# Kernel optimization log

Hardware: AMD Instinct MI355X
Metric: run time of the kernel (lower is better)

## Reference

```python
import jax, jax.numpy as jnp
import numpy as np


def setup_inputs() -> dict:
    key = jax.random.key(0)
    ks = jax.random.split(key, 4)
    C, Cb = 256, 32  # in_channels, bottleneck = C // 8
    B, H, W = 4, 64, 64
    x = jax.random.normal(ks[0], (B, C, H, W), dtype=jnp.float32)
    Wq = jax.random.normal(ks[1], (Cb, C), dtype=jnp.float32) * 0.05
    Wk = jax.random.normal(ks[2], (Cb, C), dtype=jnp.float32) * 0.05
    Wv = jax.random.normal(ks[3], (C, C), dtype=jnp.float32) * 0.05
    return {
        "x": x,
        "Wq": Wq, "bq": jnp.zeros((Cb,), jnp.float32),
        "Wk": Wk, "bk": jnp.zeros((Cb,), jnp.float32),
        "Wv": Wv, "bv": jnp.zeros((C,), jnp.float32),
    }


def reference(x, Wq, bq, Wk, bk, Wv, bv):
    B, C, H, W = x.shape
    N = H * W
    xf = x.reshape(B, C, N)  # [B, C, N]
    # 1x1 convs == channel matmuls
    q = jnp.einsum('oc,bcn->bon', Wq, xf) + bq[None, :, None]  # [B, Cb, N]
    k = jnp.einsum('oc,bcn->bon', Wk, xf) + bk[None, :, None]  # [B, Cb, N]
    v = jnp.einsum('oc,bcn->bon', Wv, xf) + bv[None, :, None]  # [B, C, N]
    # attention[b, n, m] = sum_d q[b, d, n] * k[b, d, m]
    attn = jnp.einsum('bdn,bdm->bnm', q, k)  # [B, N, N]
    attn = jax.nn.softmax(attn, axis=-1)
    # out[b, c, n] = sum_m v[b, c, m] * attn[b, m, n]
    out = jnp.einsum('bcm,bmn->bcn', v, attn).reshape(B, C, H, W)
    return out + x
```

## Files before the change

### kernel.cpp

```cpp
#include <hip/hip_runtime.h>
#include <hip/hip_bf16.h>

#define B_  4
#define C_  256
#define CB_ 32
#define N_  4096

typedef short bf16x8 __attribute__((ext_vector_type(8)));
typedef float f32x4  __attribute__((ext_vector_type(4)));
typedef float f32x16 __attribute__((ext_vector_type(16)));

static __device__ __forceinline__ bf16x8 ld_bf8(const __hip_bfloat16* p) {
    return *reinterpret_cast<const bf16x8*>(p);
}
static __device__ __forceinline__ unsigned pk2(float a, float b) {
    union { __hip_bfloat16 h[2]; unsigned u; } z;
    z.h[0] = __float2bfloat16(a); z.h[1] = __float2bfloat16(b);
    return z.u;
}


__global__ __launch_bounds__(256) void wconv(
    const float* __restrict__ Wq, const float* __restrict__ Wk,
    const float* __restrict__ Wv, __hip_bfloat16* __restrict__ Wc)
{
    int idx = (blockIdx.x * 256 + threadIdx.x) * 4;
    if (idx >= 320 * 256) return;
    int o = idx >> 8, c = idx & 255;
    const float* src = o < 32 ? Wq + o * 256 + c
                     : o < 64 ? Wk + (o - 32) * 256 + c
                              : Wv + (o - 64) * 256 + c;
    float4 f = *reinterpret_cast<const float4*>(src);
    union { __hip_bfloat16 h[4]; uint2 u; } pk;
    pk.h[0] = __float2bfloat16(f.x); pk.h[1] = __float2bfloat16(f.y);
    pk.h[2] = __float2bfloat16(f.z); pk.h[3] = __float2bfloat16(f.w);
    *reinterpret_cast<uint2*>(Wc + idx) = pk.u;
}

__global__ __launch_bounds__(256) void qkv_gemm(
    const float* __restrict__ x, const __hip_bfloat16* __restrict__ Wc,
    const float* __restrict__ bq, const float* __restrict__ bk,
    const float* __restrict__ bv,
    __hip_bfloat16* __restrict__ q8, __hip_bfloat16* __restrict__ k8,
    __hip_bfloat16* __restrict__ v8)
{
    const int b = blockIdx.y, n0 = blockIdx.x * 32;
    const int tid = threadIdx.x, lane = tid & 63, w = tid >> 6;
    const int lg = lane >> 4, lr = lane & 15;
    __shared__ __attribute__((aligned(16))) __hip_bfloat16 T[2][32][40];
    const float* xb = x + (size_t)b * C_ * N_;

    f32x4 acc[5][2] = {};
    for (int s = 0; s < 8; ++s) {
        const int c0 = s * 32, buf = s & 1;
        {
            int cl = tid >> 3, n4 = (tid & 7) * 4;
            float4 f = *reinterpret_cast<const float4*>(
                &xb[(size_t)(c0 + cl) * N_ + n0 + n4]);
            T[buf][n4 + 0][cl] = __float2bfloat16(f.x);
            T[buf][n4 + 1][cl] = __float2bfloat16(f.y);
            T[buf][n4 + 2][cl] = __float2bfloat16(f.z);
            T[buf][n4 + 3][cl] = __float2bfloat16(f.w);
        }
        __syncthreads();
        bf16x8 bfr[2];
#pragma unroll
        for (int nf = 0; nf < 2; ++nf)
            bfr[nf] = *reinterpret_cast<const bf16x8*>(&T[buf][nf * 16 + lr][lg * 8]);
#pragma unroll
        for (int t = 0; t < 5; ++t) {
            const int of = w + 4 * t;
            bf16x8 af = ld_bf8(Wc + (size_t)(of * 16 + lr) * 256 + c0 + lg * 8);
#pragma unroll
            for (int nf = 0; nf < 2; ++nf)
                acc[t][nf] = __builtin_amdgcn_mfma_f32_16x16x32_bf16(af, bfr[nf], acc[t][nf], 0, 0, 0);
        }
        __syncthreads();
    }
#pragma unroll
    for (int t = 0; t < 5; ++t) {
        const int of = w + 4 * t, ob = of * 16 + lg * 4;
        float bias[4];
#pragma unroll
        for (int i = 0; i < 4; ++i) {
            int o = ob + i;
            bias[i] = o < 32 ? bq[o] : o < 64 ? bk[o - 32] : bv[o - 64];
        }
#pragma unroll
        for (int nf = 0; nf < 2; ++nf) {
            const int n = n0 + nf * 16 + lr;
            if (ob < 64) {
                union { __hip_bfloat16 h[4]; uint2 u; } pk;
#pragma unroll
                for (int i = 0; i < 4; ++i)
                    pk.h[i] = __float2bfloat16(acc[t][nf][i] + bias[i]);
                __hip_bfloat16* dst;
                if (ob < 32)
                    dst = q8 + ((size_t)(b * 4 + (ob >> 3)) * N_ + n) * 8 + (ob & 7);
                else {
                    const int ok = ob - 32;
                    dst = k8 + ((size_t)(b * 4 + (ok >> 3)) * N_ + n) * 8 + (ok & 7);
                }
                *reinterpret_cast<uint2*>(dst) = pk.u;
            } else {
#pragma unroll
                for (int i = 0; i < 4; ++i)
                    v8[((size_t)(b * (N_ / 8) + (n >> 3)) * C_ + (ob - 64 + i)) * 8
                       + (n & 7)] = __float2bfloat16(acc[t][nf][i] + bias[i]);
            }
        }
    }
}

__global__ __launch_bounds__(256) void row_stats_part(
    const __hip_bfloat16* __restrict__ q8, const __hip_bfloat16* __restrict__ k8,
    float* __restrict__ pM, float* __restrict__ pZ)
{
    const int m0 = blockIdx.x * 64, s = blockIdx.y, b = blockIdx.z;
    const int tid = threadIdx.x, lane = tid & 63, w = tid >> 6;
    const int lg = lane >> 4, lr = lane & 15;
    const __hip_bfloat16* q8b = q8 + (size_t)b * N_ * CB_;
    const __hip_bfloat16* k8b = k8 + (size_t)b * N_ * CB_;
    const int mrow = m0 + w * 16;
    bf16x8 qf = ld_bf8(q8b + ((size_t)lg * N_ + mrow + lr) * 8);
    float rm[4] = {-1e30f, -1e30f, -1e30f, -1e30f};
    float rz[4] = {0.f, 0.f, 0.f, 0.f};
    const f32x4 zero = {0.f, 0.f, 0.f, 0.f};
    const int nbeg = s * (N_ / 4);
    for (int n = nbeg; n < nbeg + N_ / 4; n += 64) {
        f32x4 sf[4];
#pragma unroll
        for (int nf = 0; nf < 4; ++nf) {
            bf16x8 kf = ld_bf8(k8b + ((size_t)lg * N_ + n + nf * 16 + lr) * 8);
            sf[nf] = __builtin_amdgcn_mfma_f32_16x16x32_bf16(qf, kf, zero, 0, 0, 0);
        }
#pragma unroll
        for (int i = 0; i < 4; ++i) {
            float tm = fmaxf(fmaxf(sf[0][i], sf[1][i]), fmaxf(sf[2][i], sf[3][i]));
            if (tm > rm[i]) { rz[i] *= __expf(rm[i] - tm); rm[i] = tm; }
            rz[i] += __expf(sf[0][i] - rm[i]) + __expf(sf[1][i] - rm[i]) +
                     __expf(sf[2][i] - rm[i]) + __expf(sf[3][i] - rm[i]);
        }
    }
#pragma unroll
    for (int off = 1; off < 16; off <<= 1) {
#pragma unroll
        for (int i = 0; i < 4; ++i) {
            float om = __shfl_xor(rm[i], off);
            float oz = __shfl_xor(rz[i], off);
            float nm = fmaxf(rm[i], om);
            rz[i] = rz[i] * __expf(rm[i] - nm) + oz * __expf(om - nm);
            rm[i] = nm;
        }
    }
    if (lr == 0) {
        const size_t base = ((size_t)s * B_ + b) * N_ + mrow + lg * 4;
#pragma unroll
        for (int i = 0; i < 4; ++i) { pM[base + i] = rm[i]; pZ[base + i] = rz[i]; }
    }
}

__global__ __launch_bounds__(256) void stats_combine(
    const float* __restrict__ pM, const float* __restrict__ pZ,
    float* __restrict__ rowE)
{
    const int i = blockIdx.x * 256 + threadIdx.x;
    const int BN = B_ * N_;
    float m0 = pM[i], m1 = pM[BN + i], m2 = pM[2 * BN + i], m3 = pM[3 * BN + i];
    float M = fmaxf(fmaxf(m0, m1), fmaxf(m2, m3));
    float Z = pZ[i]          * __expf(m0 - M) + pZ[BN + i]     * __expf(m1 - M)
            + pZ[2 * BN + i] * __expf(m2 - M) + pZ[3 * BN + i] * __expf(m3 - M);
    rowE[i] = M + logf(Z);
}

#define PV_BODY(qC0, qC1, vC, eC, qN0, qN1, vN, eN, qpN0, qpN1, vpN0, vpN1, epN, DO_LOAD) \
  {                                                                             \
    if (DO_LOAD) {                                                              \
      qN0 = ld_bf8(qpN0); qN1 = ld_bf8(qpN1);                                   \
      _Pragma("unroll")                                                         \
      for (int ct = 0; ct < 4; ++ct) {                                          \
        vN[ct][0] = ld_bf8(vpN0 + ct * 256);                                    \
        vN[ct][1] = ld_bf8(vpN1 + ct * 256);                                    \
      }                                                                         \
      _Pragma("unroll")                                                         \
      for (int g = 0; g < 4; ++g)                                               \
        eN[g] = *reinterpret_cast<const f32x4*>(epN + 8 * g);                   \
      qpN0 += 2048; qpN1 += 2048; vpN0 += 65536; vpN1 += 65536; epN += 256;     \
    }                                                                           \
    f32x16 sf = {};                                                             \
    sf = __builtin_amdgcn_mfma_f32_32x32x16_bf16(qC0, kB0, sf, 0, 0, 0);        \
    sf = __builtin_amdgcn_mfma_f32_32x32x16_bf16(qC1, kB1, sf, 0, 0, 0);        \
    unsigned W0 = pk2(__expf(sf[0]  - eC[0][0]), __expf(sf[1]  - eC[0][1]));    \
    unsigned W1 = pk2(__expf(sf[2]  - eC[0][2]), __expf(sf[3]  - eC[0][3]));    \
    unsigned W2 = pk2(__expf(sf[4]  - eC[1][0]), __expf(sf[5]  - eC[1][1]));    \
    unsigned W3 = pk2(__expf(sf[6]  - eC[1][2]), __expf(sf[7]  - eC[1][3]));    \
    unsigned W4 = pk2(__expf(sf[8]  - eC[2][0]), __expf(sf[9]  - eC[2][1]));    \
    unsigned W5 = pk2(__expf(sf[10] - eC[2][2]), __expf(sf[11] - eC[2][3]));    \
    unsigned W6 = pk2(__expf(sf[12] - eC[3][0]), __expf(sf[13] - eC[3][1]));    \
    unsigned W7 = pk2(__expf(sf[14] - eC[3][2]), __expf(sf[15] - eC[3][3]));    \
    asm("v_permlane32_swap_b32 %0, %1" : "+v"(W0), "+v"(W2));                   \
    asm("v_permlane32_swap_b32 %0, %1" : "+v"(W1), "+v"(W3));                   \
    asm("v_permlane32_swap_b32 %0, %1" : "+v"(W4), "+v"(W6));                   \
    asm("v_permlane32_swap_b32 %0, %1" : "+v"(W5), "+v"(W7));                   \
    union { unsigned u[4]; bf16x8 v8_; } f0, f1;                                \
    f0.u[0] = W0; f0.u[1] = W1; f0.u[2] = W2; f0.u[3] = W3;                     \
    f1.u[0] = W4; f1.u[1] = W5; f1.u[2] = W6; f1.u[3] = W7;                     \
    _Pragma("unroll")                                                           \
    for (int ct = 0; ct < 4; ++ct) {                                            \
      acc[ct] = __builtin_amdgcn_mfma_f32_32x32x16_bf16(vC[ct][0], f0.v8_, acc[ct], 0, 0, 0); \
      acc[ct] = __builtin_amdgcn_mfma_f32_32x32x16_bf16(vC[ct][1], f1.v8_, acc[ct], 0, 0, 0); \
    }                                                                           \
  }

__global__ __launch_bounds__(512) void pv_attn(
    const __hip_bfloat16* __restrict__ q8, const __hip_bfloat16* __restrict__ k8,
    const __hip_bfloat16* __restrict__ v8, const float* __restrict__ rowE,
    const float* __restrict__ x, float* __restrict__ out)
{
    const int bid = blockIdx.x;
    const int xcd = bid & 7, slot = bid >> 3;
    const int b = xcd >> 1, c0 = (xcd & 1) * 128, n0 = slot * 64;
    const int tid = threadIdx.x, lane = tid & 63, w = tid >> 6;
    const int ms = w >> 1, nf = w & 1;
    const int h = lane >> 5, l31 = lane & 31;
    const __hip_bfloat16* q8b = q8 + (size_t)b * N_ * CB_;
    const __hip_bfloat16* k8b = k8 + (size_t)b * N_ * CB_;
    const __hip_bfloat16* v8b = v8 + (size_t)b * (N_ / 8) * C_ * 8;

    const int nrow = n0 + nf * 32 + l31;
    bf16x8 kB0 = ld_bf8(k8b + ((size_t)h * N_ + nrow) * 8);
    bf16x8 kB1 = ld_bf8(k8b + ((size_t)(2 + h) * N_ + nrow) * 8);

    const __hip_bfloat16* qpA0 = q8b + ((size_t)h * N_ + ms * 32 + l31) * 8;
    const __hip_bfloat16* qpA1 = q8b + ((size_t)(2 + h) * N_ + ms * 32 + l31) * 8;
    const __hip_bfloat16* qpB0 = qpA0 + 128 * 8;
    const __hip_bfloat16* qpB1 = qpA1 + 128 * 8;
    const __hip_bfloat16* vpA0 = v8b + ((size_t)(ms * 4 + h) * C_ + c0 + l31) * 8;
    const __hip_bfloat16* vpA1 = v8b + ((size_t)(ms * 4 + 2 + h) * C_ + c0 + l31) * 8;
    const __hip_bfloat16* vpB0 = vpA0 + (size_t)16 * C_ * 8;
    const __hip_bfloat16* vpB1 = vpA1 + (size_t)16 * C_ * 8;
    const float* epA = rowE + (size_t)b * N_ + 4 * h + ms * 32;
    const float* epB = epA + 128;

    f32x16 acc[4] = {};
    bf16x8 qA0, qA1, qB0, qB1;
    bf16x8 vA[4][2], vB[4][2];
    f32x4 eA[4], eB[4];

    qA0 = ld_bf8(qpA0); qA1 = ld_bf8(qpA1);
#pragma unroll
    for (int ct = 0; ct < 4; ++ct) {
        vA[ct][0] = ld_bf8(vpA0 + ct * 256);
        vA[ct][1] = ld_bf8(vpA1 + ct * 256);
    }
#pragma unroll
    for (int g = 0; g < 4; ++g)
        eA[g] = *reinterpret_cast<const f32x4*>(epA + 8 * g);
    qpA0 += 2048; qpA1 += 2048; vpA0 += 65536; vpA1 += 65536; epA += 256;

    for (int tt = 0; tt < 15; ++tt) {
        PV_BODY(qA0, qA1, vA, eA, qB0, qB1, vB, eB, qpB0, qpB1, vpB0, vpB1, epB, true)
        PV_BODY(qB0, qB1, vB, eB, qA0, qA1, vA, eA, qpA0, qpA1, vpA0, vpA1, epA, true)
    }
    PV_BODY(qA0, qA1, vA, eA, qB0, qB1, vB, eB, qpB0, qpB1, vpB0, vpB1, epB, true)
    PV_BODY(qB0, qB1, vB, eB, qA0, qA1, vA, eA, qpA0, qpA1, vpA0, vpA1, epA, false)

    __shared__ __attribute__((aligned(16))) float R[128][68];
#pragma unroll 1
    for (int p = 3; p >= 0; --p) {
        if (ms == p) {
#pragma unroll
            for (int i = 0; i < 16; ++i) {
                const int cl = (i & 3) + 8 * (i >> 2) + 4 * h;
                const int nn = nf * 32 + l31;
#pragma unroll
                for (int ct = 0; ct < 4; ++ct) {
                    if (p == 3) R[ct * 32 + cl][nn] = acc[ct][i];
                    else        R[ct * 32 + cl][nn] += acc[ct][i];
                }
            }
        }
        __syncthreads();
    }
    const int cr = tid >> 2, n16 = (tid & 3) * 16;
#pragma unroll
    for (int j = 0; j < 4; ++j) {
        f32x4 rv = *reinterpret_cast<const f32x4*>(&R[cr][n16 + 4 * j]);
        const size_t gi = ((size_t)b * C_ + c0 + cr) * N_ + n0 + n16 + 4 * j;
        f32x4 xv = *reinterpret_cast<const f32x4*>(x + gi);
        *reinterpret_cast<f32x4*>(out + gi) = rv + xv;
    }
}

extern "C" void kernel_launch(void* const* d_in, const int* in_sizes, int n_in,
                              void* d_out, int out_size, void* d_ws, size_t ws_size,
                              hipStream_t stream)
{
    const float* x  = (const float*)d_in[0];
    const float* Wq = (const float*)d_in[1];
    const float* bq = (const float*)d_in[2];
    const float* Wk = (const float*)d_in[3];
    const float* bk = (const float*)d_in[4];
    const float* Wv = (const float*)d_in[5];
    const float* bv = (const float*)d_in[6];
    float* out = (float*)d_out;

    char* ws = (char*)d_ws;
    __hip_bfloat16* Wc   = (__hip_bfloat16*)(ws);
    __hip_bfloat16* q8   = (__hip_bfloat16*)(ws + 0x040000);
    __hip_bfloat16* k8   = (__hip_bfloat16*)(ws + 0x140000);
    float*          rowE = (float*)(ws + 0x240000);
    float*          pM   = (float*)(ws + 0x250000);
    float*          pZ   = (float*)(ws + 0x290000);
    __hip_bfloat16* v8   = (__hip_bfloat16*)(ws + 0x400000);

    wconv<<<80, 256, 0, stream>>>(Wq, Wk, Wv, Wc);
    qkv_gemm<<<dim3(N_ / 32, B_), 256, 0, stream>>>(x, Wc, bq, bk, bv, q8, k8, v8);
    row_stats_part<<<dim3(N_ / 64, 4, B_), 256, 0, stream>>>(q8, k8, pM, pZ);
    stats_combine<<<B_ * N_ / 256, 256, 0, stream>>>(pM, pZ, rowE);
    pv_attn<<<512, 512, 0, stream>>>(q8, k8, v8, rowE, x, out);
}
```

Measured before the change: 135.4 us.

## Software-pipeline QK score and PV MFMAs across tiles in pv_attn

Restructures the pv_attn main loop so that each step computes QK scores for the next tile while the PV MFMAs for the previous tile's probabilities are issued. Exp and bf16 packing of one tile then overlap with matrix-core work of another. Adds a prologue and epilogue to fill and drain the pipeline, and keeps the packed probabilities live in registers between steps. It also replaces the inline-asm permlane32 swaps with the compiler builtin so the scheduler can reorder around them. The extra live registers may raise register pressure.

```diff
diff --git a/kernel.cpp b/kernel.cpp
--- a/kernel.cpp
+++ b/kernel.cpp
@@ -7,6 +7,7 @@
 #define N_  4096
 
 typedef short bf16x8 __attribute__((ext_vector_type(8)));
+typedef int   i32x2  __attribute__((ext_vector_type(2)));
 typedef float f32x4  __attribute__((ext_vector_type(4)));
 typedef float f32x16 __attribute__((ext_vector_type(16)));
 
@@ -173,8 +174,16 @@
     rowE[i] = M + logf(Z);
 }
 
-#define PV_BODY(qC0, qC1, vC, eC, qN0, qN1, vN, eN, qpN0, qpN1, vpN0, vpN1, epN, DO_LOAD) \
+#define PIPE_BODY(qC0, qC1, vP, eC, qN0, qN1, vN, eN, qpN0, qpN1, vpN0, vpN1, epN, DO_LOAD) \
   {                                                                             \
+    f32x16 sf = {};                                                             \
+    sf = __builtin_amdgcn_mfma_f32_32x32x16_bf16(qC0, kB0, sf, 0, 0, 0);        \
+    sf = __builtin_amdgcn_mfma_f32_32x32x16_bf16(qC1, kB1, sf, 0, 0, 0);        \
+    _Pragma("unroll")                                                           \
+    for (int ct = 0; ct < 4; ++ct) {                                            \
+      acc[ct] = __builtin_amdgcn_mfma_f32_32x32x16_bf16(vP[ct][0], pf0, acc[ct], 0, 0, 0); \
+      acc[ct] = __builtin_amdgcn_mfma_f32_32x32x16_bf16(vP[ct][1], pf1, acc[ct], 0, 0, 0); \
+    }                                                                           \
     if (DO_LOAD) {                                                              \
       qN0 = ld_bf8(qpN0); qN1 = ld_bf8(qpN1);                                   \
       _Pragma("unroll")                                                         \
@@ -187,9 +196,6 @@
         eN[g] = *reinterpret_cast<const f32x4*>(epN + 8 * g);                   \
       qpN0 += 2048; qpN1 += 2048; vpN0 += 65536; vpN1 += 65536; epN += 256;     \
     }                                                                           \
-    f32x16 sf = {};                                                             \
-    sf = __builtin_amdgcn_mfma_f32_32x32x16_bf16(qC0, kB0, sf, 0, 0, 0);        \
-    sf = __builtin_amdgcn_mfma_f32_32x32x16_bf16(qC1, kB1, sf, 0, 0, 0);        \
     unsigned W0 = pk2(__expf(sf[0]  - eC[0][0]), __expf(sf[1]  - eC[0][1]));    \
     unsigned W1 = pk2(__expf(sf[2]  - eC[0][2]), __expf(sf[3]  - eC[0][3]));    \
     unsigned W2 = pk2(__expf(sf[4]  - eC[1][0]), __expf(sf[5]  - eC[1][1]));    \
@@ -198,18 +204,14 @@
     unsigned W5 = pk2(__expf(sf[10] - eC[2][2]), __expf(sf[11] - eC[2][3]));    \
     unsigned W6 = pk2(__expf(sf[12] - eC[3][0]), __expf(sf[13] - eC[3][1]));    \
     unsigned W7 = pk2(__expf(sf[14] - eC[3][2]), __expf(sf[15] - eC[3][3]));    \
-    asm("v_permlane32_swap_b32 %0, %1" : "+v"(W0), "+v"(W2));                   \
-    asm("v_permlane32_swap_b32 %0, %1" : "+v"(W1), "+v"(W3));                   \
-    asm("v_permlane32_swap_b32 %0, %1" : "+v"(W4), "+v"(W6));                   \
-    asm("v_permlane32_swap_b32 %0, %1" : "+v"(W5), "+v"(W7));                   \
-    union { unsigned u[4]; bf16x8 v8_; } f0, f1;                                \
-    f0.u[0] = W0; f0.u[1] = W1; f0.u[2] = W2; f0.u[3] = W3;                     \
-    f1.u[0] = W4; f1.u[1] = W5; f1.u[2] = W6; f1.u[3] = W7;                     \
-    _Pragma("unroll")                                                           \
-    for (int ct = 0; ct < 4; ++ct) {                                            \
-      acc[ct] = __builtin_amdgcn_mfma_f32_32x32x16_bf16(vC[ct][0], f0.v8_, acc[ct], 0, 0, 0); \
-      acc[ct] = __builtin_amdgcn_mfma_f32_32x32x16_bf16(vC[ct][1], f1.v8_, acc[ct], 0, 0, 0); \
-    }                                                                           \
+    i32x2 s02 = __builtin_amdgcn_permlane32_swap((int)W0, (int)W2, false, false);\
+    i32x2 s13 = __builtin_amdgcn_permlane32_swap((int)W1, (int)W3, false, false);\
+    i32x2 s46 = __builtin_amdgcn_permlane32_swap((int)W4, (int)W6, false, false);\
+    i32x2 s57 = __builtin_amdgcn_permlane32_swap((int)W5, (int)W7, false, false);\
+    union { int u[4]; bf16x8 v8_; } f0, f1;                                     \
+    f0.u[0] = s02[0]; f0.u[1] = s13[0]; f0.u[2] = s02[1]; f0.u[3] = s13[1];     \
+    f1.u[0] = s46[0]; f1.u[1] = s57[0]; f1.u[2] = s46[1]; f1.u[3] = s57[1];     \
+    pf0 = f0.v8_; pf1 = f1.v8_;                                                 \
   }
 
 __global__ __launch_bounds__(512) void pv_attn(
@@ -246,6 +248,7 @@
     bf16x8 qA0, qA1, qB0, qB1;
     bf16x8 vA[4][2], vB[4][2];
     f32x4 eA[4], eB[4];
+    bf16x8 pf0, pf1;
 
     qA0 = ld_bf8(qpA0); qA1 = ld_bf8(qpA1);
 #pragma unroll
@@ -258,12 +261,48 @@
         eA[g] = *reinterpret_cast<const f32x4*>(epA + 8 * g);
     qpA0 += 2048; qpA1 += 2048; vpA0 += 65536; vpA1 += 65536; epA += 256;
 
-    for (int tt = 0; tt < 15; ++tt) {
-        PV_BODY(qA0, qA1, vA, eA, qB0, qB1, vB, eB, qpB0, qpB1, vpB0, vpB1, epB, true)
-        PV_BODY(qB0, qB1, vB, eB, qA0, qA1, vA, eA, qpA0, qpA1, vpA0, vpA1, epA, true)
-    }
-    PV_BODY(qA0, qA1, vA, eA, qB0, qB1, vB, eB, qpB0, qpB1, vpB0, vpB1, epB, true)
-    PV_BODY(qB0, qB1, vB, eB, qA0, qA1, vA, eA, qpA0, qpA1, vpA0, vpA1, epA, false)
+    {
+        f32x16 sf = {};
+        sf = __builtin_amdgcn_mfma_f32_32x32x16_bf16(qA0, kB0, sf, 0, 0, 0);
+        sf = __builtin_amdgcn_mfma_f32_32x32x16_bf16(qA1, kB1, sf, 0, 0, 0);
+        unsigned W0 = pk2(__expf(sf[0]  - eA[0][0]), __expf(sf[1]  - eA[0][1]));
+        unsigned W1 = pk2(__expf(sf[2]  - eA[0][2]), __expf(sf[3]  - eA[0][3]));
+        unsigned W2 = pk2(__expf(sf[4]  - eA[1][0]), __expf(sf[5]  - eA[1][1]));
+        unsigned W3 = pk2(__expf(sf[6]  - eA[1][2]), __expf(sf[7]  - eA[1][3]));
+        unsigned W4 = pk2(__expf(sf[8]  - eA[2][0]), __expf(sf[9]  - eA[2][1]));
+        unsigned W5 = pk2(__expf(sf[10] - eA[2][2]), __expf(sf[11] - eA[2][3]));
+        unsigned W6 = pk2(__expf(sf[12] - eA[3][0]), __expf(sf[13] - eA[3][1]));
+        unsigned W7 = pk2(__expf(sf[14] - eA[3][2]), __expf(sf[15] - eA[3][3]));
+        i32x2 s02 = __builtin_amdgcn_permlane32_swap((int)W0, (int)W2, false, false);
+        i32x2 s13 = __builtin_amdgcn_permlane32_swap((int)W1, (int)W3, false, false);
+        i32x2 s46 = __builtin_amdgcn_permlane32_swap((int)W4, (int)W6, false, false);
+        i32x2 s57 = __builtin_amdgcn_permlane32_swap((int)W5, (int)W7, false, false);
+        union { int u[4]; bf16x8 v8_; } f0, f1;
+        f0.u[0] = s02[0]; f0.u[1] = s13[0]; f0.u[2] = s02[1]; f0.u[3] = s13[1];
+        f1.u[0] = s46[0]; f1.u[1] = s57[0]; f1.u[2] = s46[1]; f1.u[3] = s57[1];
+        pf0 = f0.v8_; pf1 = f1.v8_;
+    }
+    qB0 = ld_bf8(qpB0); qB1 = ld_bf8(qpB1);
+#pragma unroll
+    for (int ct = 0; ct < 4; ++ct) {
+        vB[ct][0] = ld_bf8(vpB0 + ct * 256);
+        vB[ct][1] = ld_bf8(vpB1 + ct * 256);
+    }
+#pragma unroll
+    for (int g = 0; g < 4; ++g)
+        eB[g] = *reinterpret_cast<const f32x4*>(epB + 8 * g);
+    qpB0 += 2048; qpB1 += 2048; vpB0 += 65536; vpB1 += 65536; epB += 256;
+
+    for (int it = 0; it < 15; ++it) {
+        PIPE_BODY(qB0, qB1, vA, eB, qA0, qA1, vA, eA, qpA0, qpA1, vpA0, vpA1, epA, true)
+        PIPE_BODY(qA0, qA1, vB, eA, qB0, qB1, vB, eB, qpB0, qpB1, vpB0, vpB1, epB, true)
+    }
+    PIPE_BODY(qB0, qB1, vA, eB, qA0, qA1, vA, eA, qpA0, qpA1, vpA0, vpA1, epA, false)
+#pragma unroll
+    for (int ct = 0; ct < 4; ++ct) {
+        acc[ct] = __builtin_amdgcn_mfma_f32_32x32x16_bf16(vB[ct][0], pf0, acc[ct], 0, 0, 0);
+        acc[ct] = __builtin_amdgcn_mfma_f32_32x32x16_bf16(vB[ct][1], pf1, acc[ct], 0, 0, 0);
+    }
 
     __shared__ __attribute__((aligned(16))) float R[128][68];
 #pragma unroll 1
```

Result: no change. 134.5 us (-0.6%).

## Stage V tiles through double-buffered LDS in pv_attn instead of per-wave global loads

Applied to the files above, without the earlier changes.

The PV attention kernel now loads each V tile cooperatively into a 64KB double-buffered shared-memory region and has waves read their MFMA operands from LDS. Before, each wave loaded V directly from global memory and waves sharing a channel range fetched the same data. The change also swaps the bf16 pack for a byte-permute truncation and uses the permlane32_swap builtin instead of inline asm. In exchange it adds a __syncthreads per step, uses a large LDS allocation that limits occupancy, and the bf16 conversion now truncates instead of rounding.

```diff
diff --git a/kernel.cpp b/kernel.cpp
--- a/kernel.cpp
+++ b/kernel.cpp
@@ -7,6 +7,7 @@
 #define N_  4096
 
 typedef short bf16x8 __attribute__((ext_vector_type(8)));
+typedef int   i32x2  __attribute__((ext_vector_type(2)));
 typedef float f32x4  __attribute__((ext_vector_type(4)));
 typedef float f32x16 __attribute__((ext_vector_type(16)));
 
@@ -14,9 +15,8 @@
     return *reinterpret_cast<const bf16x8*>(p);
 }
 static __device__ __forceinline__ unsigned pk2(float a, float b) {
-    union { __hip_bfloat16 h[2]; unsigned u; } z;
-    z.h[0] = __float2bfloat16(a); z.h[1] = __float2bfloat16(b);
-    return z.u;
+    return __builtin_amdgcn_perm(__float_as_uint(a), __float_as_uint(b),
+                                 0x03020706u);
 }
 
 
@@ -173,23 +173,34 @@
     rowE[i] = M + logf(Z);
 }
 
-#define PV_BODY(qC0, qC1, vC, eC, qN0, qN1, vN, eN, qpN0, qpN1, vpN0, vpN1, epN, DO_LOAD) \
+#define PV_BODY(qC0, qC1, eC, qN0, qN1, eN, qpN0, qpN1, epN, DO_LOAD)          \
   {                                                                             \
+                                    \
+    bf16x8 vC[4][2];                                                            \
+    _Pragma("unroll")                                                           \
+    for (int ct = 0; ct < 4; ++ct) {                                            \
+      vC[ct][0] = *reinterpret_cast<const bf16x8*>(LB + curoff + rb0 + ct * 512);\
+      vC[ct][1] = *reinterpret_cast<const bf16x8*>(LB + curoff + rb1 + ct * 512);\
+    }                                                                           \
+        \
+    uint4 st0, st1, st2, st3;                                                   \
     if (DO_LOAD) {                                                              \
+      st0 = *reinterpret_cast<const uint4*>(vs0);                               \
+      st1 = *reinterpret_cast<const uint4*>(vs1);                               \
+      st2 = *reinterpret_cast<const uint4*>(vs2);                               \
+      st3 = *reinterpret_cast<const uint4*>(vs3);                               \
+      vs0 += 32768; vs1 += 32768; vs2 += 32768; vs3 += 32768;                   \
       qN0 = ld_bf8(qpN0); qN1 = ld_bf8(qpN1);                                   \
-      _Pragma("unroll")                                                         \
-      for (int ct = 0; ct < 4; ++ct) {                                          \
-        vN[ct][0] = ld_bf8(vpN0 + ct * 256);                                    \
-        vN[ct][1] = ld_bf8(vpN1 + ct * 256);                                    \
-      }                                                                         \
       _Pragma("unroll")                                                         \
       for (int g = 0; g < 4; ++g)                                               \
         eN[g] = *reinterpret_cast<const f32x4*>(epN + 8 * g);                   \
-      qpN0 += 2048; qpN1 += 2048; vpN0 += 65536; vpN1 += 65536; epN += 256;     \
+      qpN0 += 2048; qpN1 += 2048; epN += 256;                                   \
     }                                                                           \
+                                                                    \
     f32x16 sf = {};                                                             \
     sf = __builtin_amdgcn_mfma_f32_32x32x16_bf16(qC0, kB0, sf, 0, 0, 0);        \
     sf = __builtin_amdgcn_mfma_f32_32x32x16_bf16(qC1, kB1, sf, 0, 0, 0);        \
+                                     \
     unsigned W0 = pk2(__expf(sf[0]  - eC[0][0]), __expf(sf[1]  - eC[0][1]));    \
     unsigned W1 = pk2(__expf(sf[2]  - eC[0][2]), __expf(sf[3]  - eC[0][3]));    \
     unsigned W2 = pk2(__expf(sf[4]  - eC[1][0]), __expf(sf[5]  - eC[1][1]));    \
@@ -198,18 +209,28 @@
     unsigned W5 = pk2(__expf(sf[10] - eC[2][2]), __expf(sf[11] - eC[2][3]));    \
     unsigned W6 = pk2(__expf(sf[12] - eC[3][0]), __expf(sf[13] - eC[3][1]));    \
     unsigned W7 = pk2(__expf(sf[14] - eC[3][2]), __expf(sf[15] - eC[3][3]));    \
-    asm("v_permlane32_swap_b32 %0, %1" : "+v"(W0), "+v"(W2));                   \
-    asm("v_permlane32_swap_b32 %0, %1" : "+v"(W1), "+v"(W3));                   \
-    asm("v_permlane32_swap_b32 %0, %1" : "+v"(W4), "+v"(W6));                   \
-    asm("v_permlane32_swap_b32 %0, %1" : "+v"(W5), "+v"(W7));                   \
-    union { unsigned u[4]; bf16x8 v8_; } f0, f1;                                \
-    f0.u[0] = W0; f0.u[1] = W1; f0.u[2] = W2; f0.u[3] = W3;                     \
-    f1.u[0] = W4; f1.u[1] = W5; f1.u[2] = W6; f1.u[3] = W7;                     \
+    i32x2 s02 = __builtin_amdgcn_permlane32_swap((int)W0, (int)W2, false, false);\
+    i32x2 s13 = __builtin_amdgcn_permlane32_swap((int)W1, (int)W3, false, false);\
+    i32x2 s46 = __builtin_amdgcn_permlane32_swap((int)W4, (int)W6, false, false);\
+    i32x2 s57 = __builtin_amdgcn_permlane32_swap((int)W5, (int)W7, false, false);\
+    union { int u[4]; bf16x8 v8_; } f0, f1;                                     \
+    f0.u[0] = s02[0]; f0.u[1] = s13[0]; f0.u[2] = s02[1]; f0.u[3] = s13[1];     \
+    f1.u[0] = s46[0]; f1.u[1] = s57[0]; f1.u[2] = s46[1]; f1.u[3] = s57[1];     \
+                                                          \
     _Pragma("unroll")                                                           \
     for (int ct = 0; ct < 4; ++ct) {                                            \
       acc[ct] = __builtin_amdgcn_mfma_f32_32x32x16_bf16(vC[ct][0], f0.v8_, acc[ct], 0, 0, 0); \
       acc[ct] = __builtin_amdgcn_mfma_f32_32x32x16_bf16(vC[ct][1], f1.v8_, acc[ct], 0, 0, 0); \
     }                                                                           \
+                   \
+    if (DO_LOAD) {                                                              \
+      *reinterpret_cast<uint4*>(LB + nxtoff + wdst + 0)    = st0;               \
+      *reinterpret_cast<uint4*>(LB + nxtoff + wdst + 1024) = st1;               \
+      *reinterpret_cast<uint4*>(LB + nxtoff + wdst + 2048) = st2;               \
+      *reinterpret_cast<uint4*>(LB + nxtoff + wdst + 3072) = st3;               \
+    }                                                                           \
+    __syncthreads();                                                            \
+    { int t_ = curoff; curoff = nxtoff; nxtoff = t_; }                          \
   }
 
 __global__ __launch_bounds__(512) void pv_attn(
@@ -227,6 +248,8 @@
     const __hip_bfloat16* k8b = k8 + (size_t)b * N_ * CB_;
     const __hip_bfloat16* v8b = v8 + (size_t)b * (N_ / 8) * C_ * 8;
 
+    __shared__ __attribute__((aligned(16))) char LB[65536];
+
     const int nrow = n0 + nf * 32 + l31;
     bf16x8 kB0 = ld_bf8(k8b + ((size_t)h * N_ + nrow) * 8);
     bf16x8 kB1 = ld_bf8(k8b + ((size_t)(2 + h) * N_ + nrow) * 8);
@@ -235,37 +258,55 @@
     const __hip_bfloat16* qpA1 = q8b + ((size_t)(2 + h) * N_ + ms * 32 + l31) * 8;
     const __hip_bfloat16* qpB0 = qpA0 + 128 * 8;
     const __hip_bfloat16* qpB1 = qpA1 + 128 * 8;
-    const __hip_bfloat16* vpA0 = v8b + ((size_t)(ms * 4 + h) * C_ + c0 + l31) * 8;
-    const __hip_bfloat16* vpA1 = v8b + ((size_t)(ms * 4 + 2 + h) * C_ + c0 + l31) * 8;
-    const __hip_bfloat16* vpB0 = vpA0 + (size_t)16 * C_ * 8;
-    const __hip_bfloat16* vpB1 = vpA1 + (size_t)16 * C_ * 8;
     const float* epA = rowE + (size_t)b * N_ + 4 * h + ms * 32;
     const float* epB = epA + 128;
 
+    const __hip_bfloat16* vs0;
+    const __hip_bfloat16* vs1;
+    const __hip_bfloat16* vs2;
+    const __hip_bfloat16* vs3;
+    {
+        const int i0 = w * 4;
+        vs0 = v8b + ((size_t)((i0 + 0) >> 1) * C_ + c0 + ((i0 + 0) & 1) * 64 + lane) * 8;
+        vs1 = v8b + ((size_t)((i0 + 1) >> 1) * C_ + c0 + ((i0 + 1) & 1) * 64 + lane) * 8;
+        vs2 = v8b + ((size_t)((i0 + 2) >> 1) * C_ + c0 + ((i0 + 2) & 1) * 64 + lane) * 8;
+        vs3 = v8b + ((size_t)((i0 + 3) >> 1) * C_ + c0 + ((i0 + 3) & 1) * 64 + lane) * 8;
+    }
+    const int wdst = w * 4096 + lane * 16;
+    const int rb0 = (ms * 4 + h) * 2048 + l31 * 16;
+    const int rb1 = (ms * 4 + 2 + h) * 2048 + l31 * 16;
+    int curoff = 0, nxtoff = 32768;
+
     f32x16 acc[4] = {};
     bf16x8 qA0, qA1, qB0, qB1;
-    bf16x8 vA[4][2], vB[4][2];
     f32x4 eA[4], eB[4];
 
-    qA0 = ld_bf8(qpA0); qA1 = ld_bf8(qpA1);
-#pragma unroll
-    for (int ct = 0; ct < 4; ++ct) {
-        vA[ct][0] = ld_bf8(vpA0 + ct * 256);
-        vA[ct][1] = ld_bf8(vpA1 + ct * 256);
-    }
-#pragma unroll
-    for (int g = 0; g < 4; ++g)
-        eA[g] = *reinterpret_cast<const f32x4*>(epA + 8 * g);
-    qpA0 += 2048; qpA1 += 2048; vpA0 += 65536; vpA1 += 65536; epA += 256;
-
-    for (int tt = 0; tt < 15; ++tt) {
-        PV_BODY(qA0, qA1, vA, eA, qB0, qB1, vB, eB, qpB0, qpB1, vpB0, vpB1, epB, true)
-        PV_BODY(qB0, qB1, vB, eB, qA0, qA1, vA, eA, qpA0, qpA1, vpA0, vpA1, epA, true)
-    }
-    PV_BODY(qA0, qA1, vA, eA, qB0, qB1, vB, eB, qpB0, qpB1, vpB0, vpB1, epB, true)
-    PV_BODY(qB0, qB1, vB, eB, qA0, qA1, vA, eA, qpA0, qpA1, vpA0, vpA1, epA, false)
-
-    __shared__ __attribute__((aligned(16))) float R[128][68];
+    {
+        uint4 s0 = *reinterpret_cast<const uint4*>(vs0);
+        uint4 s1 = *reinterpret_cast<const uint4*>(vs1);
+        uint4 s2 = *reinterpret_cast<const uint4*>(vs2);
+        uint4 s3 = *reinterpret_cast<const uint4*>(vs3);
+        vs0 += 32768; vs1 += 32768; vs2 += 32768; vs3 += 32768;
+        qA0 = ld_bf8(qpA0); qA1 = ld_bf8(qpA1);
+#pragma unroll
+        for (int g = 0; g < 4; ++g)
+            eA[g] = *reinterpret_cast<const f32x4*>(epA + 8 * g);
+        qpA0 += 2048; qpA1 += 2048; epA += 256;
+        *reinterpret_cast<uint4*>(LB + wdst + 0)    = s0;
+        *reinterpret_cast<uint4*>(LB + wdst + 1024) = s1;
+        *reinterpret_cast<uint4*>(LB + wdst + 2048) = s2;
+        *reinterpret_cast<uint4*>(LB + wdst + 3072) = s3;
+    }
+    __syncthreads();
+
+    for (int it = 0; it < 15; ++it) {
+        PV_BODY(qA0, qA1, eA, qB0, qB1, eB, qpB0, qpB1, epB, true)
+        PV_BODY(qB0, qB1, eB, qA0, qA1, eA, qpA0, qpA1, epA, true)
+    }
+    PV_BODY(qA0, qA1, eA, qB0, qB1, eB, qpB0, qpB1, epB, true)
+    PV_BODY(qB0, qB1, eB, qA0, qA1, eA, qpA0, qpA1, epA, false)
+
+    float (*R)[68] = reinterpret_cast<float (*)[68]>(LB);
 #pragma unroll 1
     for (int p = 3; p >= 0; --p) {
         if (ms == p) {
```

After: 142.7 us. +5.4%, slower.
